# Kernel optimization log

Measured on AMD Instinct MI355X. Metric: run time of the kernel, lower is better.

Reference implementation:

```python
import jax, jax.numpy as jnp
import numpy as np
from jax import lax

F8 = jnp.float8_e4m3fn


def setup_inputs() -> dict:
    key = jax.random.key(0)
    kx, kw = jax.random.split(key)
    x = jax.random.normal(kx, (2, 128, 4, 192, 320), dtype=jnp.float32)
    # matches reset_parameters: normal(0, 0.02) then cast to fp8
    weight = jax.random.normal(kw, (128, 128, 3, 3, 3), dtype=jnp.float32) * 0.02
    return {"x": x, "weight": weight}


def reference(x, weight):
    # fp8 e4m3 quantization round-trip (the torch module stores/consumes fp8),
    # compute/accumulate in fp32 as an fp8 conv kernel would.
    xq = x.astype(F8).astype(jnp.float32)
    wq = weight.astype(F8).astype(jnp.float32)
    # causal temporal padding: (kT-1, 0) = (2, 0); spatial 'same' padding (1,1)
    xp = jnp.pad(xq, ((0, 0), (0, 0), (2, 0), (1, 1), (1, 1)))
    out = lax.conv_general_dilated(
        xp, wq,
        window_strides=(1, 1, 1),
        padding='VALID',
        dimension_numbers=('NCDHW', 'OIDHW', 'NCDHW'),
    )  # (B, 128, 4, 192, 320)
    return out
```

## Files before the change

### kernel.cpp

```cpp
#include <hip/hip_runtime.h>
#include <hip/hip_fp8.h>


using f32x4 = __attribute__((ext_vector_type(4))) float;
typedef long long i64;
struct alignas(16) L2v { i64 x, y; };

namespace {
constexpr int Cc = 128, Dd = 4, Hh = 192, Ww = 320;
constexpr int HP = 194, WP = 322;
constexpr int NTAP = 27;
constexpr size_t PLANE = (size_t)16 * WP * 8;
constexpr size_t XQ_BYTES = (size_t)2 * Dd * HP * PLANE;
constexpr int ZA = 8 * 2 * 2576;
constexpr int ZB = 8 * 192 * 32;
}

__global__ __launch_bounds__(256) void zero_pad_kernel(unsigned char* __restrict__ xq) {
  int i = blockIdx.x * 256 + threadIdx.x;
  if (i < ZA) {
    int bd = i / (2 * 2576);
    int r = i - bd * (2 * 2576);
    int hsel = r / 2576, seg = r - hsel * 2576;
    L2v z{0, 0};
    *(L2v*)(xq + ((size_t)bd * HP + (hsel ? 193 : 0)) * PLANE + (size_t)seg * 16) = z;
  } else if (i < ZA + ZB) {
    int j = i - ZA;
    int bd = j / (192 * 32);
    int r = j - bd * (192 * 32);
    int h = r / 32 + 1;
    int t = r & 31;
    int g = t >> 1, wsel = t & 1;
    *(i64*)(xq + ((size_t)bd * HP + h) * PLANE + (size_t)g * WP * 8
            + (size_t)(wsel ? 321 : 0) * 8) = 0;
  }
}

__global__ __launch_bounds__(256) void qx_kernel(const float* __restrict__ x,
                                                 unsigned char* __restrict__ xq) {
  __shared__ unsigned char lt[64 * 132];
  const int tid = threadIdx.x;
  const int b = blockIdx.z >> 2, d = blockIdx.z & 3;
  const int h = blockIdx.y;
  const int w0 = blockIdx.x * 64;
  const int wl = tid & 63, cig = tid >> 6;
  const size_t cstr = (size_t)Dd * Hh * Ww;
  const float* xp = x + (((size_t)b * Cc * Dd + d) * Hh + h) * Ww + w0 + wl;
  #pragma unroll 4
  for (int i = 0; i < 32; ++i) {
    int ci = cig * 32 + i;
    __hip_fp8_e4m3 q(xp[ci * cstr]);
    lt[wl * 132 + ci] = q.__x;
  }
  __syncthreads();
  unsigned char* plane = xq + ((size_t)(b * Dd + d) * HP + h + 1) * PLANE;
  #pragma unroll
  for (int k = 0; k < 2; ++k) {
    int i = tid + k * 256;
    int g = i >> 5;
    int wp = (i & 31) * 2;
    i64 lo = *(const i64*)(lt + wp * 132 + g * 8);
    i64 hi = *(const i64*)(lt + (wp + 1) * 132 + g * 8);
    L2v v{lo, hi};
    *(L2v*)(plane + (size_t)g * WP * 8 + (size_t)(w0 + 1 + wp) * 8) = v;
  }
}

__global__ void wpack_kernel(const float* __restrict__ w, unsigned char* __restrict__ wpk) {
  int idx = blockIdx.x * 256 + threadIdx.x;
  if (idx >= Cc * Cc * NTAP) return;
  int tap = idx % NTAP;
  int t = idx / NTAP;
  int ci = t % Cc, co = t / Cc;
  int wv = co >> 5, mf = (co >> 4) & 1, l15 = co & 15;
  __hip_fp8_e4m3 q(w[idx]);
  wpk[((((size_t)tap * 16 + (ci >> 3)) * 4 + wv) * 16 + l15) * 16 + mf * 8 + (ci & 7)] = q.__x;
}

__global__ __launch_bounds__(256, 4) void conv_mfma(const unsigned char* __restrict__ xq,
                                                    const unsigned char* __restrict__ wpk,
                                                    float* __restrict__ out) {
  __shared__ unsigned char lb[48 * 528];
  const int tid = threadIdx.x;
  const int lane = tid & 63, wv = tid >> 6;
  const int l15 = lane & 15, kg = lane >> 4;
  const int b = blockIdx.z >> 2, dout = blockIdx.z & 3;
  const int h0 = blockIdx.y * 2;
  const int w0 = blockIdx.x * 64;
  const int kdmin = dout >= 2 ? 0 : 2 - dout;
  const int aoff = kg * 1024 + wv * 256 + l15 * 16;

  f32x4 acc[2][2][4];
  #pragma unroll
  for (int a = 0; a < 2; ++a)
    #pragma unroll
    for (int m = 0; m < 2; ++m)
      #pragma unroll
      for (int n = 0; n < 4; ++n) acc[a][m][n] = (f32x4){0.f, 0.f, 0.f, 0.f};

  for (int cc = 0; cc < 4; ++cc) {
    __syncthreads();
    for (int i = tid + kdmin * 528; i < 48 * 33; i += 256) {
      int row = i / 33, seg = i - row * 33;
      int g = row & 3, hrow = (row >> 2) & 3, kd = row >> 4;
      const unsigned char* src = xq
          + ((size_t)(b * Dd + dout + kd - 2) * HP + h0 + hrow) * PLANE
          + (size_t)(cc * 4 + g) * WP * 8 + (size_t)w0 * 8 + (size_t)seg * 16;
      *(L2v*)(lb + row * 528 + seg * 16) = *(const L2v*)src;
    }
    __syncthreads();
    __builtin_amdgcn_s_setprio(1);
    const unsigned char* wcc = wpk + cc * 4096 + aoff;
    for (int kd = kdmin; kd < 3; ++kd) {
      const unsigned char* wb = wcc + (size_t)kd * 9 * 16384;
      const unsigned char* lbase = lb + (kd * 16 + kg) * 528 + l15 * 8;
      L2v av[9];
      #pragma unroll
      for (int t = 0; t < 9; ++t) av[t] = *(const L2v*)(wb + (size_t)t * 16384);
      #pragma unroll
      for (int kh = 0; kh < 3; ++kh)
        #pragma unroll
        for (int hr = 0; hr < 2; ++hr)
          #pragma unroll
          for (int kw = 0; kw < 3; ++kw)
            #pragma unroll
            for (int nf = 0; nf < 4; ++nf) {
              i64 bf = *(const i64*)(lbase + (hr + kh) * 2112 + kw * 8 + nf * 128);
              acc[hr][0][nf] = __builtin_amdgcn_mfma_f32_16x16x32_fp8_fp8(
                  av[kh * 3 + kw].x, bf, acc[hr][0][nf], 0, 0, 0);
              acc[hr][1][nf] = __builtin_amdgcn_mfma_f32_16x16x32_fp8_fp8(
                  av[kh * 3 + kw].y, bf, acc[hr][1][nf], 0, 0, 0);
            }
    }
    __builtin_amdgcn_s_setprio(0);
  }

  #pragma unroll
  for (int hr = 0; hr < 2; ++hr)
    #pragma unroll
    for (int mf = 0; mf < 2; ++mf)
      #pragma unroll
      for (int nf = 0; nf < 4; ++nf) {
        int ww = w0 + nf * 16 + l15;
        #pragma unroll
        for (int r = 0; r < 4; ++r) {
          int co = wv * 32 + mf * 16 + kg * 4 + r;
          out[(((size_t)b * Cc + co) * Dd + dout) * (size_t)(Hh * Ww)
              + (size_t)(h0 + hr) * Ww + ww] = acc[hr][mf][nf][r];
        }
      }
}

extern "C" void kernel_launch(void* const* d_in, const int* in_sizes, int n_in,
                              void* d_out, int out_size, void* d_ws, size_t ws_size,
                              hipStream_t stream) {
  const float* x = (const float*)d_in[0];
  const float* w = (const float*)d_in[1];
  unsigned char* xq = (unsigned char*)d_ws;
  unsigned char* wpk = xq + XQ_BYTES;
  float* out = (float*)d_out;

  int nz = ZA + ZB;
  zero_pad_kernel<<<(nz + 255) / 256, 256, 0, stream>>>(xq);

  dim3 g1(Ww / 64, Hh, 2 * Dd);
  qx_kernel<<<g1, 256, 0, stream>>>(x, xq);

  int nw = Cc * Cc * NTAP;
  wpack_kernel<<<(nw + 255) / 256, 256, 0, stream>>>(w, wpk);

  dim3 g2(Ww / 64, Hh / 2, 2 * Dd);
  conv_mfma<<<g2, 256, 0, stream>>>(xq, wpk, out);
}
```

Measured before the change: 265.3 us.

## Switch conv to 32x32x64 scaled fp8 MFMA with 32-channel grouped layout

New measurement: 247.6 us. -6.7%, faster.

```diff
diff --git a/kernel.cpp b/kernel.cpp
--- a/kernel.cpp
+++ b/kernel.cpp
@@ -2,7 +2,8 @@
 #include <hip/hip_fp8.h>
 
 
-using f32x4 = __attribute__((ext_vector_type(4))) float;
+using f32x16 = __attribute__((ext_vector_type(16))) float;
+using i32x8 = __attribute__((ext_vector_type(8))) int;
 typedef long long i64;
 struct alignas(16) L2v { i64 x, y; };
 
@@ -10,10 +11,11 @@
 constexpr int Cc = 128, Dd = 4, Hh = 192, Ww = 320;
 constexpr int HP = 194, WP = 322;
 constexpr int NTAP = 27;
-constexpr size_t PLANE = (size_t)16 * WP * 8;
+constexpr size_t PLANE = (size_t)4 * WP * 32;
 constexpr size_t XQ_BYTES = (size_t)2 * Dd * HP * PLANE;
 constexpr int ZA = 8 * 2 * 2576;
 constexpr int ZB = 8 * 192 * 32;
+constexpr int GSTR = WP * 32;
 }
 
 __global__ __launch_bounds__(256) void zero_pad_kernel(unsigned char* __restrict__ xq) {
@@ -30,15 +32,16 @@
     int r = j - bd * (192 * 32);
     int h = r / 32 + 1;
     int t = r & 31;
-    int g = t >> 1, wsel = t & 1;
-    *(i64*)(xq + ((size_t)bd * HP + h) * PLANE + (size_t)g * WP * 8
-            + (size_t)(wsel ? 321 : 0) * 8) = 0;
+    int g = t >> 3, s2 = t & 7;
+    int wsel = s2 >> 2, part = s2 & 3;
+    *(i64*)(xq + ((size_t)bd * HP + h) * PLANE + (size_t)g * GSTR
+            + (size_t)(wsel ? 321 : 0) * 32 + part * 8) = 0;
   }
 }
 
 __global__ __launch_bounds__(256) void qx_kernel(const float* __restrict__ x,
                                                  unsigned char* __restrict__ xq) {
-  __shared__ unsigned char lt[64 * 132];
+  __shared__ unsigned char lt[64 * 136];
   const int tid = threadIdx.x;
   const int b = blockIdx.z >> 2, d = blockIdx.z & 3;
   const int h = blockIdx.y;
@@ -50,19 +53,18 @@
   for (int i = 0; i < 32; ++i) {
     int ci = cig * 32 + i;
     __hip_fp8_e4m3 q(xp[ci * cstr]);
-    lt[wl * 132 + ci] = q.__x;
+    lt[wl * 136 + ci] = q.__x;
   }
   __syncthreads();
   unsigned char* plane = xq + ((size_t)(b * Dd + d) * HP + h + 1) * PLANE;
-  #pragma unroll
-  for (int k = 0; k < 2; ++k) {
-    int i = tid + k * 256;
-    int g = i >> 5;
-    int wp = (i & 31) * 2;
-    i64 lo = *(const i64*)(lt + wp * 132 + g * 8);
-    i64 hi = *(const i64*)(lt + (wp + 1) * 132 + g * 8);
-    L2v v{lo, hi};
-    *(L2v*)(plane + (size_t)g * WP * 8 + (size_t)(w0 + 1 + wp) * 8) = v;
+  {
+    int g = tid >> 6, w = tid & 63;
+    const unsigned char* src = lt + w * 136 + g * 32;
+    i64 a0 = *(const i64*)(src), a1 = *(const i64*)(src + 8);
+    i64 a2 = *(const i64*)(src + 16), a3 = *(const i64*)(src + 24);
+    unsigned char* dst = plane + (size_t)g * GSTR + (size_t)(w0 + 1 + w) * 32;
+    *(L2v*)dst = L2v{a0, a1};
+    *(L2v*)(dst + 16) = L2v{a2, a3};
   }
 }
 
@@ -72,83 +74,103 @@
   int tap = idx % NTAP;
   int t = idx / NTAP;
   int ci = t % Cc, co = t / Cc;
-  int wv = co >> 5, mf = (co >> 4) & 1, l15 = co & 15;
+  int cc = ci >> 6, ct = co >> 5;
+  int lane = (((ci >> 5) & 1) << 5) | (co & 31);
   __hip_fp8_e4m3 q(w[idx]);
-  wpk[((((size_t)tap * 16 + (ci >> 3)) * 4 + wv) * 16 + l15) * 16 + mf * 8 + (ci & 7)] = q.__x;
+  wpk[((((size_t)tap * 2 + cc) * 4 + ct) * 64 + lane) * 32 + (ci & 31)] = q.__x;
 }
 
-__global__ __launch_bounds__(256, 4) void conv_mfma(const unsigned char* __restrict__ xq,
+__global__ __launch_bounds__(256, 3) void conv_mfma(const unsigned char* __restrict__ xq,
                                                     const unsigned char* __restrict__ wpk,
                                                     float* __restrict__ out) {
-  __shared__ unsigned char lb[48 * 528];
+  __shared__ unsigned char lb[24 * 2112];
   const int tid = threadIdx.x;
   const int lane = tid & 63, wv = tid >> 6;
-  const int l15 = lane & 15, kg = lane >> 4;
+  const int l31 = lane & 31, chalf = lane >> 5;
+  const int hr = wv >> 1, ch = wv & 1;
   const int b = blockIdx.z >> 2, dout = blockIdx.z & 3;
   const int h0 = blockIdx.y * 2;
   const int w0 = blockIdx.x * 64;
   const int kdmin = dout >= 2 ? 0 : 2 - dout;
-  const int aoff = kg * 1024 + wv * 256 + l15 * 16;
 
-  f32x4 acc[2][2][4];
+  f32x16 acc[2][2];
   #pragma unroll
   for (int a = 0; a < 2; ++a)
     #pragma unroll
-    for (int m = 0; m < 2; ++m)
+    for (int n = 0; n < 2; ++n)
       #pragma unroll
-      for (int n = 0; n < 4; ++n) acc[a][m][n] = (f32x4){0.f, 0.f, 0.f, 0.f};
+      for (int r = 0; r < 16; ++r) acc[a][n][r] = 0.f;
 
-  for (int cc = 0; cc < 4; ++cc) {
+  for (int cc = 0; cc < 2; ++cc) {
     __syncthreads();
-    for (int i = tid + kdmin * 528; i < 48 * 33; i += 256) {
-      int row = i / 33, seg = i - row * 33;
-      int g = row & 3, hrow = (row >> 2) & 3, kd = row >> 4;
+    for (int u = tid + kdmin * 528; u < 1584; u += 256) {
+      int w = u % 66;
+      int rest = u / 66;
+      int chf = rest & 1, rest2 = rest >> 1;
+      int hrow = rest2 & 3, kd = rest2 >> 2;
       const unsigned char* src = xq
           + ((size_t)(b * Dd + dout + kd - 2) * HP + h0 + hrow) * PLANE
-          + (size_t)(cc * 4 + g) * WP * 8 + (size_t)w0 * 8 + (size_t)seg * 16;
-      *(L2v*)(lb + row * 528 + seg * 16) = *(const L2v*)src;
+          + (size_t)(cc * 2 + chf) * GSTR + (size_t)(w0 + w) * 32;
+      L2v lo = *(const L2v*)src;
+      L2v hi = *(const L2v*)(src + 16);
+      int t = (w >> 2) & 1;
+      unsigned char* base = lb + rest * 2112;
+      *(L2v*)(base + (2 * w + t) * 16) = lo;
+      *(L2v*)(base + (2 * w + 1 - t) * 16) = hi;
     }
     __syncthreads();
     __builtin_amdgcn_s_setprio(1);
-    const unsigned char* wcc = wpk + cc * 4096 + aoff;
     for (int kd = kdmin; kd < 3; ++kd) {
-      const unsigned char* wb = wcc + (size_t)kd * 9 * 16384;
-      const unsigned char* lbase = lb + (kd * 16 + kg) * 528 + l15 * 8;
-      L2v av[9];
       #pragma unroll
-      for (int t = 0; t < 9; ++t) av[t] = *(const L2v*)(wb + (size_t)t * 16384);
-      #pragma unroll
-      for (int kh = 0; kh < 3; ++kh)
+      for (int kh = 0; kh < 3; ++kh) {
+        i32x8 av[3][2];
         #pragma unroll
-        for (int hr = 0; hr < 2; ++hr)
+        for (int kw = 0; kw < 3; ++kw)
           #pragma unroll
-          for (int kw = 0; kw < 3; ++kw)
+          for (int ct = 0; ct < 2; ++ct) {
+            const unsigned char* ap = wpk +
+                ((((size_t)(kd * 9 + kh * 3 + kw) * 2 + cc) * 4 + ch * 2 + ct) * 64 + lane) * 32;
+            int4 alo = *(const int4*)ap;
+            int4 ahi = *(const int4*)(ap + 16);
+            av[kw][ct][0] = alo.x; av[kw][ct][1] = alo.y;
+            av[kw][ct][2] = alo.z; av[kw][ct][3] = alo.w;
+            av[kw][ct][4] = ahi.x; av[kw][ct][5] = ahi.y;
+            av[kw][ct][6] = ahi.z; av[kw][ct][7] = ahi.w;
+          }
+        const unsigned char* pbase = lb + (((kd * 4 + hr + kh) * 2 + chalf)) * 2112;
+        #pragma unroll
+        for (int kw = 0; kw < 3; ++kw)
+          #pragma unroll
+          for (int nf = 0; nf < 2; ++nf) {
+            int wl = nf * 32 + l31 + kw;
+            int t = (wl >> 2) & 1;
+            int4 blo = *(const int4*)(pbase + (2 * wl + t) * 16);
+            int4 bhi = *(const int4*)(pbase + (2 * wl + 1 - t) * 16);
+            i32x8 bv;
+            bv[0] = blo.x; bv[1] = blo.y; bv[2] = blo.z; bv[3] = blo.w;
+            bv[4] = bhi.x; bv[5] = bhi.y; bv[6] = bhi.z; bv[7] = bhi.w;
             #pragma unroll
-            for (int nf = 0; nf < 4; ++nf) {
-              i64 bf = *(const i64*)(lbase + (hr + kh) * 2112 + kw * 8 + nf * 128);
-              acc[hr][0][nf] = __builtin_amdgcn_mfma_f32_16x16x32_fp8_fp8(
-                  av[kh * 3 + kw].x, bf, acc[hr][0][nf], 0, 0, 0);
-              acc[hr][1][nf] = __builtin_amdgcn_mfma_f32_16x16x32_fp8_fp8(
-                  av[kh * 3 + kw].y, bf, acc[hr][1][nf], 0, 0, 0);
-            }
+            for (int ct = 0; ct < 2; ++ct)
+              acc[ct][nf] = __builtin_amdgcn_mfma_scale_f32_32x32x64_f8f6f4(
+                  av[kw][ct], bv, acc[ct][nf], 0, 0, 0, 127, 0, 127);
+          }
+      }
     }
     __builtin_amdgcn_s_setprio(0);
   }
 
   #pragma unroll
-  for (int hr = 0; hr < 2; ++hr)
+  for (int ct = 0; ct < 2; ++ct)
     #pragma unroll
-    for (int mf = 0; mf < 2; ++mf)
+    for (int nf = 0; nf < 2; ++nf) {
+      int ww = w0 + nf * 32 + l31;
       #pragma unroll
-      for (int nf = 0; nf < 4; ++nf) {
-        int ww = w0 + nf * 16 + l15;
-        #pragma unroll
-        for (int r = 0; r < 4; ++r) {
-          int co = wv * 32 + mf * 16 + kg * 4 + r;
-          out[(((size_t)b * Cc + co) * Dd + dout) * (size_t)(Hh * Ww)
-              + (size_t)(h0 + hr) * Ww + ww] = acc[hr][mf][nf][r];
-        }
+      for (int reg = 0; reg < 16; ++reg) {
+        int co = ch * 64 + ct * 32 + (reg & 3) + 8 * (reg >> 2) + 4 * chalf;
+        out[(((size_t)b * Cc + co) * Dd + dout) * (size_t)(Hh * Ww)
+            + (size_t)(h0 + hr) * Ww + ww] = acc[ct][nf][reg];
       }
+    }
 }
 
 extern "C" void kernel_launch(void* const* d_in, const int* in_sizes, int n_in,
```
